# Kernel optimization log

Measured on AMD Instinct MI355X. Metric: run time of the kernel, lower is better.

## Reference

```python
import jax, jax.numpy as jnp
import numpy as np

N_EMBD = 1024
N_HEADS = 16
HEAD_SIZE = N_EMBD // N_HEADS
B, T = 2, 2048


def setup_inputs() -> dict:
    key = jax.random.key(0)
    ks = jax.random.split(key, 6)
    s_in = 1.0 / np.sqrt(N_EMBD)
    x = jax.random.normal(ks[0], (B, T, N_EMBD), dtype=jnp.float32)
    # per-head projection weights, stored (H, C, Dh) = x @ W per head
    wq = jax.random.uniform(ks[1], (N_HEADS, N_EMBD, HEAD_SIZE), dtype=jnp.float32, minval=-s_in, maxval=s_in)
    wk = jax.random.uniform(ks[2], (N_HEADS, N_EMBD, HEAD_SIZE), dtype=jnp.float32, minval=-s_in, maxval=s_in)
    wv = jax.random.uniform(ks[3], (N_HEADS, N_EMBD, HEAD_SIZE), dtype=jnp.float32, minval=-s_in, maxval=s_in)
    # output projection (in, out) layout plus bias
    w_proj = jax.random.uniform(ks[4], (N_EMBD, N_EMBD), dtype=jnp.float32, minval=-s_in, maxval=s_in)
    b_proj = jax.random.uniform(ks[5], (N_EMBD,), dtype=jnp.float32, minval=-s_in, maxval=s_in)
    return {"x": x, "wq": wq, "wk": wk, "wv": wv, "w_proj": w_proj, "b_proj": b_proj}


def reference(x, wq, wk, wv, w_proj, b_proj):
    Bb, Tt, C = x.shape
    # all-head QKV projections in one einsum each: (B,T,C)x(H,C,Dh)->(B,H,T,Dh)
    q = jnp.einsum('btc,hcd->bhtd', x, wq)
    k = jnp.einsum('btc,hcd->bhtd', x, wk)
    v = jnp.einsum('btc,hcd->bhtd', x, wv)
    # NOTE: original scales by C**-0.5 with C = full n_embd, not head_size
    scores = jnp.einsum('bhtd,bhsd->bhts', q, k) * (C ** -0.5)
    causal = jnp.tril(jnp.ones((Tt, Tt), dtype=bool))  # is_decoder=True
    scores = jnp.where(causal, scores, -jnp.inf)
    wei = jax.nn.softmax(scores, axis=-1)
    out = jnp.einsum('bhts,bhsd->bhtd', wei, v)
    # concat heads: (B,H,T,Dh) -> (B,T,H*Dh)
    out = out.transpose(0, 2, 1, 3).reshape(Bb, Tt, C)
    return out @ w_proj + b_proj
```

## Files before the change

kernel.cpp:

```cpp
#include <hip/hip_runtime.h>


typedef unsigned short u16;
typedef unsigned int u32;

using bf16x8 = __attribute__((ext_vector_type(8))) short;
using bf16x4 = __attribute__((ext_vector_type(4))) short;
using f32x4  = __attribute__((ext_vector_type(4))) float;

#define T_SEQ 2048
#define C_DIM 1024
#define H_NUM 16
#define D_HEAD 64
#define NSEG 41

static __device__ inline f32x4 mfma16(bf16x8 a, bf16x8 b, f32x4 c) {
  return __builtin_amdgcn_mfma_f32_16x16x32_bf16(a, b, c, 0, 0, 0);
}

static __device__ inline short f2bf(float f) {
  union { float f; u32 u; } v; v.f = f;
  u32 u = v.u;
  return (short)((u + 0x7FFFu + ((u >> 16) & 1u)) >> 16);
}

static __device__ inline float bf2f(short s) {
  union { u32 u; float f; } v; v.u = ((u32)(u16)s) << 16;
  return v.f;
}

static __device__ inline float exp2_hw(float x) {
  return __builtin_amdgcn_exp2f(x);
}

static __device__ inline u32 cvtpk_bf16(float a, float b) {
  u32 r;
  asm("v_cvt_pk_bf16_f32 %0, %1, %2" : "=v"(r) : "v"(a), "v"(b));
  return r;
}

static __device__ inline void gload_lds16(const short* g, short* l) {
  __builtin_amdgcn_global_load_lds(
      (const __attribute__((address_space(1))) unsigned int*)g,
      (__attribute__((address_space(3))) unsigned int*)l,
      16, 0, 0);
}

__global__ __launch_bounds__(256) void ingest_kernel(
    const float* __restrict__ x, const float* __restrict__ wq,
    const float* __restrict__ wk, const float* __restrict__ wv,
    const float* __restrict__ wproj,
    short* __restrict__ xb, short* __restrict__ wt, short* __restrict__ wpT) {
  const int bid = blockIdx.x, t = threadIdx.x;
  if (bid < 4096) {
    size_t i4 = ((size_t)bid * 256 + t) * 4;
    const float4 v = *(const float4*)(x + i4);
    bf16x4 o4;
    o4[0] = f2bf(v.x); o4[1] = f2bf(v.y); o4[2] = f2bf(v.z); o4[3] = f2bf(v.w);
    *(bf16x4*)(xb + i4) = o4;
    return;
  }
  __shared__ short lt[64][72];
  const int rl = t >> 2, q16 = (t & 3) * 16;
  if (bid < 4864) {
    const int wb = bid - 4096;
    const int h3 = wb >> 4, c0 = (wb & 15) * 64;
    const float* w = (h3 < 16) ? wq : (h3 < 32) ? wk : wv;
    const int h = h3 & 15;
    const float* rp = w + (size_t)h * 65536 + (size_t)(c0 + rl) * 64 + q16;
#pragma unroll
    for (int j = 0; j < 16; j++) lt[rl][q16 + j] = f2bf(rp[j]);
    __syncthreads();
    short* op = wt + (size_t)h3 * 65536 + (size_t)rl * 1024 + c0 + q16;
#pragma unroll
    for (int j = 0; j < 16; j++) op[j] = lt[q16 + j][rl];
  } else {
    const int wc = bid - 4864;
    const int k0 = (wc >> 4) * 64, n0 = (wc & 15) * 64;
    const float* rp = wproj + (size_t)(k0 + rl) * 1024 + n0 + q16;
#pragma unroll
    for (int j = 0; j < 16; j++) lt[rl][q16 + j] = f2bf(rp[j]);
    __syncthreads();
    short* op = wpT + (size_t)(n0 + rl) * 1024 + k0 + q16;
#pragma unroll
    for (int j = 0; j < 16; j++) op[j] = lt[q16 + j][rl];
  }
}

__global__ __launch_bounds__(256) void qkv_kernel(
    const short* __restrict__ x, const short* __restrict__ wt,
    short* __restrict__ qo, short* __restrict__ ko, short* __restrict__ vto) {
  const int m0 = blockIdx.x * 128;
  const int n0 = blockIdx.y * 128;
  const int tid = threadIdx.x, w = tid >> 6, lane = tid & 63;
  const int l15 = lane & 15, quad = lane >> 4;
  const int wm = w >> 1, wn = w & 1;

  __shared__ __align__(16) short As[2][128 * 32];
  __shared__ __align__(16) short Bs[2][128 * 32];

  const int srow = w * 32 + (lane >> 2);
  const int skof = (lane & 3) * 8;
  const short* ga0 = x  + (size_t)(m0 + srow) * 1024 + skof;
  const short* ga1 = ga0 + 16 * 1024;
  const short* gb0 = wt + (size_t)(n0 + srow) * 1024 + skof;
  const short* gb1 = gb0 + 16 * 1024;
  const int lof0 = (w * 32) * 32;
  const int lof1 = (w * 32 + 16) * 32;

  f32x4 acc[4][4];
#pragma unroll
  for (int i = 0; i < 4; i++)
#pragma unroll
    for (int j = 0; j < 4; j++) acc[i][j] = f32x4{0, 0, 0, 0};

  const bool isv = (n0 >= 2048);

  auto stage = [&](int bi, int kt) {
    const int k0 = kt * 32;
    gload_lds16(ga0 + k0, &As[bi][lof0]);
    gload_lds16(ga1 + k0, &As[bi][lof1]);
    gload_lds16(gb0 + k0, &Bs[bi][lof0]);
    gload_lds16(gb1 + k0, &Bs[bi][lof1]);
  };
  auto compute = [&](int bi) {
    const short* ard = &As[bi][(wm * 64 + l15) * 32 + quad * 8];
    const short* brd = &Bs[bi][(wn * 64 + l15) * 32 + quad * 8];
    bf16x8 af[4], bfr[4];
#pragma unroll
    for (int i = 0; i < 4; i++) {
      af[i]  = *(const bf16x8*)(ard + i * 16 * 32);
      bfr[i] = *(const bf16x8*)(brd + i * 16 * 32);
    }
    if (!isv) {
#pragma unroll
      for (int mi = 0; mi < 4; mi++)
#pragma unroll
        for (int ni = 0; ni < 4; ni++)
          acc[mi][ni] = mfma16(af[mi], bfr[ni], acc[mi][ni]);
    } else {
#pragma unroll
      for (int ni = 0; ni < 4; ni++)
#pragma unroll
        for (int mi = 0; mi < 4; mi++)
          acc[ni][mi] = mfma16(bfr[ni], af[mi], acc[ni][mi]);
    }
  };

  stage(0, 0);
  __syncthreads();
#pragma unroll 1
  for (int kt2 = 0; kt2 < 16; kt2++) {
    stage(1, 2 * kt2 + 1);
    compute(0);
    __syncthreads();
    if (kt2 < 15) stage(0, 2 * kt2 + 2);
    compute(1);
    __syncthreads();
  }

  const int chunk = (n0 >> 6) + wn;
  const int sel = chunk >> 4, h = chunk & 15;
  if (!isv) {
    short* outp = (sel == 0) ? qo : ko;
    const float sc = (sel == 0) ? 0.045084441f : 1.0f;
#pragma unroll
    for (int mi = 0; mi < 4; mi++) {
#pragma unroll
      for (int r = 0; r < 4; r++) {
        int tg = m0 + wm * 64 + mi * 16 + quad * 4 + r;
        int b = tg >> 11, tl = tg & 2047;
        size_t rowb = ((size_t)(b * H_NUM + h) * T_SEQ + tl) * D_HEAD;
#pragma unroll
        for (int ni = 0; ni < 4; ni++)
          outp[rowb + ni * 16 + l15] = f2bf(acc[mi][ni][r] * sc);
      }
    }
  } else {
#pragma unroll
    for (int ni = 0; ni < 4; ni++) {
#pragma unroll
      for (int r = 0; r < 4; r++) {
        int d = ni * 16 + quad * 4 + r;
#pragma unroll
        for (int mi = 0; mi < 4; mi++) {
          int tg = m0 + wm * 64 + mi * 16 + l15;
          int b = tg >> 11, tl = tg & 2047;
          vto[((size_t)(b * H_NUM + h) * D_HEAD + d) * T_SEQ + tl] =
              f2bf(acc[ni][mi][r]);
        }
      }
    }
  }
}

__global__ __launch_bounds__(128) void attn_part_kernel(
    const short* __restrict__ q, const short* __restrict__ k,
    const short* __restrict__ vt, short* __restrict__ po,
    float* __restrict__ pl) {
  static const unsigned char cst[33] = {
      0, 3, 5, 7, 9, 11, 12, 14, 15, 16, 17, 18, 19, 21, 22, 23, 24,
      25, 26, 27, 28, 29, 30, 31, 32, 34, 35, 36, 37, 38, 39, 40, 41};
  static const unsigned char seg_qtb[NSEG] = {
      0, 1, 2, 2, 3, 3, 4, 4, 5, 5, 6, 6, 6, 7, 7, 8, 8, 9, 9, 9,
      10, 10, 10, 11, 11, 11, 12, 12, 12, 13, 13, 13, 13, 14, 14, 14, 14,
      15, 15, 15, 15};
  static const unsigned short seg_s0[NSEG] = {
      0, 0, 0, 192, 0, 384, 0, 448, 0, 384, 0, 192, 768, 0, 448, 0, 576,
      0, 576, 1152, 0, 384, 896, 0, 512, 1024, 0, 576, 1152, 0, 576, 1152,
      1664, 0, 384, 896, 1408, 0, 512, 1024, 1536};
  static const unsigned char seg_nt[NSEG] = {
      2, 4, 3, 3, 6, 2, 7, 3, 6, 6, 3, 9, 2, 7, 9, 9, 9, 9, 9, 2,
      6, 8, 8, 8, 8, 8, 9, 9, 8, 9, 9, 8, 2, 6, 8, 8, 8, 8, 8, 8, 8};

  const int id = blockIdx.x;
  const int hb = id & 31;
  const int p  = id >> 5;
  const int pair = p & 1, chunk = p >> 1;

  const size_t bh = (size_t)hb;
  const short* qp = q  + bh * T_SEQ * D_HEAD;
  const short* kp = k  + bh * T_SEQ * D_HEAD;
  const short* vp = vt + bh * D_HEAD * T_SEQ;

  const int tid = threadIdx.x;
  const int wid = tid >> 6;
  const int lane = tid & 63;
  const int l15 = lane & 15, quad = lane >> 4;
  const int w4 = pair * 2 + wid;

  __shared__ __align__(16) short P_lds[2][32][72];
  short (*pq)[72] = P_lds[wid];

  const int sfirst = cst[chunk], slast = cst[chunk + 1];
#pragma unroll 1
  for (int si = sfirst; si < slast; ++si) {
    const int qtb = seg_qtb[si];
    const int sbeg = seg_s0[si];
    const int send = sbeg + seg_nt[si] * 64;
    const int q0w = qtb * 128 + w4 * 32;
    const int s_hi = min(send, ((q0w + 95) >> 6) << 6);

    bf16x8 qa[2][2];
#pragma unroll
    for (int h2 = 0; h2 < 2; h2++)
#pragma unroll
      for (int c2 = 0; c2 < 2; c2++)
        qa[h2][c2] = *(const bf16x8*)(qp + (size_t)(q0w + h2 * 16 + l15) * D_HEAD
                                      + c2 * 32 + quad * 8);

    f32x4 o[2][4];
#pragma unroll
    for (int h2 = 0; h2 < 2; h2++)
#pragma unroll
      for (int c = 0; c < 4; c++) o[h2][c] = f32x4{0, 0, 0, 0};
    float l_i[2] = { 0.f, 0.f };

    bf16x8 ka[4][2];
#pragma unroll
    for (int c = 0; c < 4; c++) {
      const short* krow = kp + (size_t)(sbeg + c * 16 + l15) * D_HEAD + quad * 8;
      ka[c][0] = *(const bf16x8*)(krow);
      ka[c][1] = *(const bf16x8*)(krow + 32);
    }

#pragma unroll 1
    for (int s0 = sbeg; s0 < s_hi; s0 += 64) {
      bf16x8 va[2][4];
#pragma unroll
      for (int kb2 = 0; kb2 < 2; kb2++)
#pragma unroll
        for (int c = 0; c < 4; c++)
          va[kb2][c] = *(const bf16x8*)(vp + (size_t)(c * 16 + l15) * T_SEQ
                                        + s0 + kb2 * 32 + quad * 8);

      f32x4 s[2][4];
      __builtin_amdgcn_s_setprio(1);
#pragma unroll
      for (int c = 0; c < 4; c++) {
#pragma unroll
        for (int h2 = 0; h2 < 2; h2++) {
          f32x4 z = { 0, 0, 0, 0 };
          z = mfma16(ka[c][0], qa[h2][0], z);
          z = mfma16(ka[c][1], qa[h2][1], z);
          s[h2][c] = z;
        }
      }
      __builtin_amdgcn_s_setprio(0);

      const int s0n = (s0 + 64 < s_hi) ? (s0 + 64) : s0;
#pragma unroll
      for (int c = 0; c < 4; c++) {
        const short* krow = kp + (size_t)(s0n + c * 16 + l15) * D_HEAD + quad * 8;
        ka[c][0] = *(const bf16x8*)(krow);
        ka[c][1] = *(const bf16x8*)(krow + 32);
      }

      const bool needMask = (s0 + 64 > q0w);
#pragma unroll
      for (int h2 = 0; h2 < 2; h2++) {
        const int qg = q0w + h2 * 16 + l15;
        if (needMask) {
#pragma unroll
          for (int c = 0; c < 4; c++)
#pragma unroll
            for (int r = 0; r < 4; r++)
              if (s0 + c * 16 + quad * 4 + r > qg) s[h2][c][r] = -1e30f;
        }
        float rs = 0.f;
#pragma unroll
        for (int c = 0; c < 4; c++) {
#pragma unroll
          for (int r = 0; r < 4; r++) {
            float p2 = exp2_hw(s[h2][c][r]);
            s[h2][c][r] = p2;
            rs += p2;
          }
        }
        l_i[h2] += rs;
#pragma unroll
        for (int c = 0; c < 4; c++) {
          uint2 pw;
          pw.x = cvtpk_bf16(s[h2][c][0], s[h2][c][1]);
          pw.y = cvtpk_bf16(s[h2][c][2], s[h2][c][3]);
          *(uint2*)(&pq[h2 * 16 + l15][c * 16 + quad * 4]) = pw;
        }
      }
      asm volatile("" ::: "memory");

      __builtin_amdgcn_s_setprio(1);
#pragma unroll
      for (int kb2 = 0; kb2 < 2; kb2++) {
        bf16x8 pb[2];
        pb[0] = *(const bf16x8*)(&pq[l15][kb2 * 32 + quad * 8]);
        pb[1] = *(const bf16x8*)(&pq[16 + l15][kb2 * 32 + quad * 8]);
#pragma unroll
        for (int c = 0; c < 4; c++) {
          o[0][c] = mfma16(va[kb2][c], pb[0], o[0][c]);
          o[1][c] = mfma16(va[kb2][c], pb[1], o[1][c]);
        }
      }
      __builtin_amdgcn_s_setprio(0);
      asm volatile("" ::: "memory");
    }

    const size_t prow = (bh * NSEG + si) * 128;
#pragma unroll
    for (int h2 = 0; h2 < 2; h2++) {
      float lsum = l_i[h2];
      lsum += __shfl_xor(lsum, 16);
      lsum += __shfl_xor(lsum, 32);
      float inv = (lsum > 0.f) ? 1.0f / lsum : 0.f;
      int qlocal = w4 * 32 + h2 * 16 + l15;
      size_t rowoff = (prow + qlocal) * 64;
#pragma unroll
      for (int c = 0; c < 4; c++) {
        uint2 ow;
        ow.x = cvtpk_bf16(o[h2][c][0] * inv, o[h2][c][1] * inv);
        ow.y = cvtpk_bf16(o[h2][c][2] * inv, o[h2][c][3] * inv);
        *(uint2*)(&po[rowoff + c * 16 + quad * 4]) = ow;
      }
      if (quad == 0) pl[prow + qlocal] = lsum;
    }
  }
}

__global__ __launch_bounds__(256) void attn_merge_kernel(
    const short* __restrict__ po, const float* __restrict__ pl,
    short* __restrict__ attnb) {
  static const unsigned char mseg0[16] = {0, 1, 2, 4, 6, 8, 10, 13,
                                          15, 17, 20, 23, 26, 29, 33, 37};
  static const unsigned char mcnt[16]  = {1, 1, 2, 2, 2, 2, 3, 2,
                                          2, 3, 3, 3, 3, 4, 4, 4};
  int id = blockIdx.x * 256 + threadIdx.x;
  int dg = id & 7;
  int h  = (id >> 3) & 15;
  int t  = (id >> 7) & 2047;
  int b  = id >> 18;
  int qtb = t >> 7, ql = t & 127;
  int nch = mcnt[qtb];
  size_t bh = (size_t)(b * H_NUM + h);
  size_t r0 = (bh * NSEG + mseg0[qtb]) * 128 + ql;
  bf16x8 res;
  if (nch == 1) {
    res = *(const bf16x8*)(po + r0 * 64 + dg * 8);
  } else {
    float acc[8] = {0, 0, 0, 0, 0, 0, 0, 0};
    float lsum = 0.f;
    for (int c = 0; c < nch; c++) {
      size_t r = r0 + (size_t)c * 128;
      float lc = pl[r];
      lsum += lc;
      bf16x8 p = *(const bf16x8*)(po + r * 64 + dg * 8);
#pragma unroll
      for (int j = 0; j < 8; j++) acc[j] += lc * bf2f(p[j]);
    }
    float inv = 1.0f / lsum;
#pragma unroll
    for (int j = 0; j < 8; j++) res[j] = f2bf(acc[j] * inv);
  }
  *(bf16x8*)(&attnb[((size_t)(b * T_SEQ + t)) * C_DIM + h * D_HEAD + dg * 8]) = res;
}

__global__ __launch_bounds__(256) void proj_kernel(
    const short* __restrict__ a_in, const short* __restrict__ wpT,
    const float* __restrict__ bias, float* __restrict__ out) {
  const int m0 = blockIdx.x * 128;
  const int n0 = blockIdx.y * 128;
  const int tid = threadIdx.x, w = tid >> 6, lane = tid & 63;
  const int l15 = lane & 15, quad = lane >> 4;
  const int wm = w >> 1, wn = w & 1;

  __shared__ __align__(16) short As[2][128 * 32];
  __shared__ __align__(16) short Bs[2][128 * 32];

  const int srow = w * 32 + (lane >> 2);
  const int skof = (lane & 3) * 8;
  const short* ga0 = a_in + (size_t)(m0 + srow) * 1024 + skof;
  const short* ga1 = ga0 + 16 * 1024;
  const short* gb0 = wpT + (size_t)(n0 + srow) * 1024 + skof;
  const short* gb1 = gb0 + 16 * 1024;
  const int lof0 = (w * 32) * 32;
  const int lof1 = (w * 32 + 16) * 32;

  f32x4 acc[4][4];
#pragma unroll
  for (int i = 0; i < 4; i++)
#pragma unroll
    for (int j = 0; j < 4; j++) acc[i][j] = f32x4{0, 0, 0, 0};

  auto stage = [&](int bi, int kt) {
    const int k0 = kt * 32;
    gload_lds16(ga0 + k0, &As[bi][lof0]);
    gload_lds16(ga1 + k0, &As[bi][lof1]);
    gload_lds16(gb0 + k0, &Bs[bi][lof0]);
    gload_lds16(gb1 + k0, &Bs[bi][lof1]);
  };
  auto compute = [&](int bi) {
    const short* ard = &As[bi][(wm * 64 + l15) * 32 + quad * 8];
    const short* brd = &Bs[bi][(wn * 64 + l15) * 32 + quad * 8];
    bf16x8 af[4], bfr[4];
#pragma unroll
    for (int i = 0; i < 4; i++) {
      af[i]  = *(const bf16x8*)(ard + i * 16 * 32);
      bfr[i] = *(const bf16x8*)(brd + i * 16 * 32);
    }
#pragma unroll
    for (int mi = 0; mi < 4; mi++)
#pragma unroll
      for (int ni = 0; ni < 4; ni++)
        acc[mi][ni] = mfma16(af[mi], bfr[ni], acc[mi][ni]);
  };

  stage(0, 0);
  __syncthreads();
#pragma unroll 1
  for (int kt2 = 0; kt2 < 16; kt2++) {
    stage(1, 2 * kt2 + 1);
    compute(0);
    __syncthreads();
    if (kt2 < 15) stage(0, 2 * kt2 + 2);
    compute(1);
    __syncthreads();
  }

#pragma unroll
  for (int mi = 0; mi < 4; mi++) {
#pragma unroll
    for (int r = 0; r < 4; r++) {
      int mq = m0 + wm * 64 + mi * 16 + quad * 4 + r;
#pragma unroll
      for (int ni = 0; ni < 4; ni++) {
        int n = n0 + wn * 64 + ni * 16 + l15;
        out[(size_t)mq * C_DIM + n] = acc[mi][ni][r] + bias[n];
      }
    }
  }
}

extern "C" void kernel_launch(void* const* d_in, const int* in_sizes, int n_in,
                              void* d_out, int out_size, void* d_ws, size_t ws_size,
                              hipStream_t stream) {
  const float* x     = (const float*)d_in[0];
  const float* wq    = (const float*)d_in[1];
  const float* wk    = (const float*)d_in[2];
  const float* wv    = (const float*)d_in[3];
  const float* wproj = (const float*)d_in[4];
  const float* bias  = (const float*)d_in[5];

  short* ws = (short*)d_ws;
  short* wpT    = ws;
  short* qb     = ws + 1048576;
  short* wt_qkv = ws + 9437184;
  short* xb     = ws + 12582912;
  short* po     = ws + 5242880;
  float* pl     = (float*)(ws + 15990784);
  short* attnb  = ws + 1048576;
  short* kb     = (short*)d_out;
  short* vtb    = (short*)d_out + 4194304;

  ingest_kernel<<<5120, 256, 0, stream>>>(x, wq, wk, wv, wproj, xb, wt_qkv, wpT);
  qkv_kernel<<<dim3(32, 24), 256, 0, stream>>>(xb, wt_qkv, qb, kb, vtb);
  attn_part_kernel<<<2048, 128, 0, stream>>>(qb, kb, vtb, po, pl);
  attn_merge_kernel<<<2048, 256, 0, stream>>>(po, pl, attnb);
  proj_kernel<<<dim3(32, 8), 256, 0, stream>>>(attnb, wpT, bias, (float*)d_out);
}
```

Measured before the change: 232.5 us.

## Stage K/V tiles in shared memory across four waves with uniform 512-key chunks

The attention-partial kernel now runs 4-wave blocks that cover a whole 128-query tile. Each 64-key K and V tile is loaded into swizzled LDS with direct global-to-LDS loads and shared by all waves, where before each wave fetched K and V from global memory itself. The split into work items changes from a hand-tuned segment table to fixed 512-key chunks, dispatched in a heavy-first order, and the merge kernel's indexing is updated to match. This cuts redundant global K/V traffic, at the cost of two block barriers per tile and less per-wave freedom to run independently.

```diff
diff --git a/kernel.cpp b/kernel.cpp
--- a/kernel.cpp
+++ b/kernel.cpp
@@ -12,7 +12,7 @@
 #define C_DIM 1024
 #define H_NUM 16
 #define D_HEAD 64
-#define NSEG 41
+#define NCHUNK 40
 
 static __device__ inline f32x4 mfma16(bf16x8 a, bf16x8 b, f32x4 c) {
   return __builtin_amdgcn_mfma_f32_16x16x32_bf16(a, b, c, 0, 0, 0);
@@ -194,29 +194,29 @@
   }
 }
 
-__global__ __launch_bounds__(128) void attn_part_kernel(
+__global__ __launch_bounds__(256) void attn_part_kernel(
     const short* __restrict__ q, const short* __restrict__ k,
     const short* __restrict__ vt, short* __restrict__ po,
     float* __restrict__ pl) {
-  static const unsigned char cst[33] = {
-      0, 3, 5, 7, 9, 11, 12, 14, 15, 16, 17, 18, 19, 21, 22, 23, 24,
-      25, 26, 27, 28, 29, 30, 31, 32, 34, 35, 36, 37, 38, 39, 40, 41};
-  static const unsigned char seg_qtb[NSEG] = {
-      0, 1, 2, 2, 3, 3, 4, 4, 5, 5, 6, 6, 6, 7, 7, 8, 8, 9, 9, 9,
-      10, 10, 10, 11, 11, 11, 12, 12, 12, 13, 13, 13, 13, 14, 14, 14, 14,
+  static const unsigned char order[NCHUNK] = {
+      3, 4, 6, 8, 10, 11, 12, 13, 15, 16, 18, 19, 21, 22, 23, 24, 25, 26,
+      28, 29, 30, 32, 33, 34, 36, 37, 38, 39,
+      2, 9, 20, 35,
+      1, 7, 17, 31,
+      0, 5, 14, 27};
+  static const unsigned char qtb_of[NCHUNK] = {
+      0, 1, 2, 3, 4, 4, 5, 5, 6, 6, 7, 7, 8, 8, 8, 9, 9, 9, 10, 10,
+      10, 11, 11, 11, 12, 12, 12, 12, 13, 13, 13, 13, 14, 14, 14, 14,
       15, 15, 15, 15};
-  static const unsigned short seg_s0[NSEG] = {
-      0, 0, 0, 192, 0, 384, 0, 448, 0, 384, 0, 192, 768, 0, 448, 0, 576,
-      0, 576, 1152, 0, 384, 896, 0, 512, 1024, 0, 576, 1152, 0, 576, 1152,
-      1664, 0, 384, 896, 1408, 0, 512, 1024, 1536};
-  static const unsigned char seg_nt[NSEG] = {
-      2, 4, 3, 3, 6, 2, 7, 3, 6, 6, 3, 9, 2, 7, 9, 9, 9, 9, 9, 2,
-      6, 8, 8, 8, 8, 8, 9, 9, 8, 9, 9, 8, 2, 6, 8, 8, 8, 8, 8, 8, 8};
-
+  static const unsigned char base16[16] = {0, 1, 2, 3, 4, 6, 8, 10,
+                                           12, 15, 18, 21, 24, 28, 32, 36};
   const int id = blockIdx.x;
   const int hb = id & 31;
   const int p  = id >> 5;
-  const int pair = p & 1, chunk = p >> 1;
+  const int pblk = order[p];
+  const int qtb = qtb_of[pblk];
+  const int sbeg = (pblk - base16[qtb]) * 512;
+  const int send = min(sbeg + 512, (qtb + 1) * 128);
 
   const size_t bh = (size_t)hb;
   const short* qp = q  + bh * T_SEQ * D_HEAD;
@@ -224,163 +224,163 @@
   const short* vp = vt + bh * D_HEAD * T_SEQ;
 
   const int tid = threadIdx.x;
-  const int wid = tid >> 6;
+  const int w4 = tid >> 6;
   const int lane = tid & 63;
   const int l15 = lane & 15, quad = lane >> 4;
-  const int w4 = pair * 2 + wid;
-
-  __shared__ __align__(16) short P_lds[2][32][72];
-  short (*pq)[72] = P_lds[wid];
-
-  const int sfirst = cst[chunk], slast = cst[chunk + 1];
+  const int swz8 = (l15 & 7) * 8;
+
+  __shared__ __align__(16) short Ks[4096];
+  __shared__ __align__(16) short Vs[4096];
+  __shared__ __align__(16) short Ps[4][2048];
+  short* pp = Ps[w4];
+
+  const int q0w = qtb * 128 + w4 * 32;
+  const int s_hi = min(send, ((qtb * 128 + 96 + 95) >> 6) << 6);
+
+  const int srow = w4 * 16 + (lane >> 3);
+  const int scol = ((lane & 7) ^ (lane >> 3)) * 8;
+  const short* gK0 = kp + (size_t)(sbeg + srow) * 64 + scol;
+  const short* gK1 = kp + (size_t)(sbeg + srow + 8) * 64 + scol;
+  const short* gV0 = vp + (size_t)srow * 2048 + sbeg + scol;
+  const short* gV1 = vp + (size_t)(srow + 8) * 2048 + sbeg + scol;
+  short* lK0 = Ks + w4 * 1024 + lane * 8;
+  short* lK1 = Ks + w4 * 1024 + 512 + lane * 8;
+  short* lV0 = Vs + w4 * 1024 + lane * 8;
+  short* lV1 = Vs + w4 * 1024 + 512 + lane * 8;
+
+  auto stageKV = [&](int toff) {
+    gload_lds16(gK0 + (size_t)toff * 64, lK0);
+    gload_lds16(gK1 + (size_t)toff * 64, lK1);
+    gload_lds16(gV0 + toff, lV0);
+    gload_lds16(gV1 + toff, lV1);
+  };
+
+  const int rbase = l15 * 64;
+  const int koff0 = (quad * 8) ^ swz8;
+  const int koff1 = (32 + quad * 8) ^ swz8;
+
+  bf16x8 qa[2][2];
+#pragma unroll
+  for (int h2 = 0; h2 < 2; h2++)
+#pragma unroll
+    for (int c2 = 0; c2 < 2; c2++)
+      qa[h2][c2] = *(const bf16x8*)(qp + (size_t)(q0w + h2 * 16 + l15) * D_HEAD
+                                    + c2 * 32 + quad * 8);
+
+  f32x4 o[2][4];
+#pragma unroll
+  for (int h2 = 0; h2 < 2; h2++)
+#pragma unroll
+    for (int c = 0; c < 4; c++) o[h2][c] = f32x4{0, 0, 0, 0};
+  float l_i[2] = { 0.f, 0.f };
+
+  stageKV(0);
+
 #pragma unroll 1
-  for (int si = sfirst; si < slast; ++si) {
-    const int qtb = seg_qtb[si];
-    const int sbeg = seg_s0[si];
-    const int send = sbeg + seg_nt[si] * 64;
-    const int q0w = qtb * 128 + w4 * 32;
-    const int s_hi = min(send, ((q0w + 95) >> 6) << 6);
-
-    bf16x8 qa[2][2];
-#pragma unroll
-    for (int h2 = 0; h2 < 2; h2++)
-#pragma unroll
-      for (int c2 = 0; c2 < 2; c2++)
-        qa[h2][c2] = *(const bf16x8*)(qp + (size_t)(q0w + h2 * 16 + l15) * D_HEAD
-                                      + c2 * 32 + quad * 8);
-
-    f32x4 o[2][4];
-#pragma unroll
-    for (int h2 = 0; h2 < 2; h2++)
-#pragma unroll
-      for (int c = 0; c < 4; c++) o[h2][c] = f32x4{0, 0, 0, 0};
-    float l_i[2] = { 0.f, 0.f };
-
-    bf16x8 ka[4][2];
+  for (int s0 = sbeg; s0 < s_hi; s0 += 64) {
+    __syncthreads();
+
+    f32x4 s[2][4];
+    __builtin_amdgcn_s_setprio(1);
 #pragma unroll
     for (int c = 0; c < 4; c++) {
-      const short* krow = kp + (size_t)(sbeg + c * 16 + l15) * D_HEAD + quad * 8;
-      ka[c][0] = *(const bf16x8*)(krow);
-      ka[c][1] = *(const bf16x8*)(krow + 32);
-    }
-
-#pragma unroll 1
-    for (int s0 = sbeg; s0 < s_hi; s0 += 64) {
-      bf16x8 va[2][4];
-#pragma unroll
-      for (int kb2 = 0; kb2 < 2; kb2++)
+      bf16x8 k0 = *(const bf16x8*)(Ks + c * 1024 + rbase + koff0);
+      bf16x8 k1 = *(const bf16x8*)(Ks + c * 1024 + rbase + koff1);
+#pragma unroll
+      for (int h2 = 0; h2 < 2; h2++) {
+        f32x4 z = { 0, 0, 0, 0 };
+        z = mfma16(k0, qa[h2][0], z);
+        z = mfma16(k1, qa[h2][1], z);
+        s[h2][c] = z;
+      }
+    }
+    __builtin_amdgcn_s_setprio(0);
+
+    const bool needMask = (s0 + 64 > q0w);
+#pragma unroll
+    for (int h2 = 0; h2 < 2; h2++) {
+      const int qg = q0w + h2 * 16 + l15;
+      if (needMask) {
 #pragma unroll
         for (int c = 0; c < 4; c++)
-          va[kb2][c] = *(const bf16x8*)(vp + (size_t)(c * 16 + l15) * T_SEQ
-                                        + s0 + kb2 * 32 + quad * 8);
-
-      f32x4 s[2][4];
-      __builtin_amdgcn_s_setprio(1);
+#pragma unroll
+          for (int r = 0; r < 4; r++)
+            if (s0 + c * 16 + quad * 4 + r > qg) s[h2][c][r] = -1e30f;
+      }
+      float rs = 0.f;
 #pragma unroll
       for (int c = 0; c < 4; c++) {
 #pragma unroll
-        for (int h2 = 0; h2 < 2; h2++) {
-          f32x4 z = { 0, 0, 0, 0 };
-          z = mfma16(ka[c][0], qa[h2][0], z);
-          z = mfma16(ka[c][1], qa[h2][1], z);
-          s[h2][c] = z;
+        for (int r = 0; r < 4; r++) {
+          float p2 = exp2_hw(s[h2][c][r]);
+          s[h2][c][r] = p2;
+          rs += p2;
         }
       }
-      __builtin_amdgcn_s_setprio(0);
-
-      const int s0n = (s0 + 64 < s_hi) ? (s0 + 64) : s0;
+      l_i[h2] += rs;
 #pragma unroll
       for (int c = 0; c < 4; c++) {
-        const short* krow = kp + (size_t)(s0n + c * 16 + l15) * D_HEAD + quad * 8;
-        ka[c][0] = *(const bf16x8*)(krow);
-        ka[c][1] = *(const bf16x8*)(krow + 32);
-      }
-
-      const bool needMask = (s0 + 64 > q0w);
-#pragma unroll
-      for (int h2 = 0; h2 < 2; h2++) {
-        const int qg = q0w + h2 * 16 + l15;
-        if (needMask) {
-#pragma unroll
-          for (int c = 0; c < 4; c++)
-#pragma unroll
-            for (int r = 0; r < 4; r++)
-              if (s0 + c * 16 + quad * 4 + r > qg) s[h2][c][r] = -1e30f;
-        }
-        float rs = 0.f;
-#pragma unroll
-        for (int c = 0; c < 4; c++) {
-#pragma unroll
-          for (int r = 0; r < 4; r++) {
-            float p2 = exp2_hw(s[h2][c][r]);
-            s[h2][c][r] = p2;
-            rs += p2;
-          }
-        }
-        l_i[h2] += rs;
-#pragma unroll
-        for (int c = 0; c < 4; c++) {
-          uint2 pw;
-          pw.x = cvtpk_bf16(s[h2][c][0], s[h2][c][1]);
-          pw.y = cvtpk_bf16(s[h2][c][2], s[h2][c][3]);
-          *(uint2*)(&pq[h2 * 16 + l15][c * 16 + quad * 4]) = pw;
-        }
-      }
-      asm volatile("" ::: "memory");
-
-      __builtin_amdgcn_s_setprio(1);
-#pragma unroll
-      for (int kb2 = 0; kb2 < 2; kb2++) {
-        bf16x8 pb[2];
-        pb[0] = *(const bf16x8*)(&pq[l15][kb2 * 32 + quad * 8]);
-        pb[1] = *(const bf16x8*)(&pq[16 + l15][kb2 * 32 + quad * 8]);
-#pragma unroll
-        for (int c = 0; c < 4; c++) {
-          o[0][c] = mfma16(va[kb2][c], pb[0], o[0][c]);
-          o[1][c] = mfma16(va[kb2][c], pb[1], o[1][c]);
-        }
-      }
-      __builtin_amdgcn_s_setprio(0);
-      asm volatile("" ::: "memory");
-    }
-
-    const size_t prow = (bh * NSEG + si) * 128;
-#pragma unroll
-    for (int h2 = 0; h2 < 2; h2++) {
-      float lsum = l_i[h2];
-      lsum += __shfl_xor(lsum, 16);
-      lsum += __shfl_xor(lsum, 32);
-      float inv = (lsum > 0.f) ? 1.0f / lsum : 0.f;
-      int qlocal = w4 * 32 + h2 * 16 + l15;
-      size_t rowoff = (prow + qlocal) * 64;
+        uint2 pw;
+        pw.x = cvtpk_bf16(s[h2][c][0], s[h2][c][1]);
+        pw.y = cvtpk_bf16(s[h2][c][2], s[h2][c][3]);
+        *(uint2*)(pp + (h2 * 16 + l15) * 64 + ((c * 16 + quad * 4) ^ swz8)) = pw;
+      }
+    }
+    asm volatile("" ::: "memory");
+
+    __builtin_amdgcn_s_setprio(1);
+#pragma unroll
+    for (int kb2 = 0; kb2 < 2; kb2++) {
+      const int ko = kb2 ? koff1 : koff0;
+      bf16x8 pb0 = *(const bf16x8*)(pp + rbase + ko);
+      bf16x8 pb1 = *(const bf16x8*)(pp + 1024 + rbase + ko);
 #pragma unroll
       for (int c = 0; c < 4; c++) {
-        uint2 ow;
-        ow.x = cvtpk_bf16(o[h2][c][0] * inv, o[h2][c][1] * inv);
-        ow.y = cvtpk_bf16(o[h2][c][2] * inv, o[h2][c][3] * inv);
-        *(uint2*)(&po[rowoff + c * 16 + quad * 4]) = ow;
-      }
-      if (quad == 0) pl[prow + qlocal] = lsum;
-    }
+        bf16x8 va = *(const bf16x8*)(Vs + c * 1024 + rbase + ko);
+        o[0][c] = mfma16(va, pb0, o[0][c]);
+        o[1][c] = mfma16(va, pb1, o[1][c]);
+      }
+    }
+    __builtin_amdgcn_s_setprio(0);
+
+    __syncthreads();
+    if (s0 + 64 < s_hi) stageKV(s0 + 64 - sbeg);
+  }
+
+  const size_t prow = (bh * NCHUNK + pblk) * 128;
+#pragma unroll
+  for (int h2 = 0; h2 < 2; h2++) {
+    float lsum = l_i[h2];
+    lsum += __shfl_xor(lsum, 16);
+    lsum += __shfl_xor(lsum, 32);
+    float inv = (lsum > 0.f) ? 1.0f / lsum : 0.f;
+    int qlocal = w4 * 32 + h2 * 16 + l15;
+    size_t rowoff = (prow + qlocal) * 64;
+#pragma unroll
+    for (int c = 0; c < 4; c++) {
+      uint2 ow;
+      ow.x = cvtpk_bf16(o[h2][c][0] * inv, o[h2][c][1] * inv);
+      ow.y = cvtpk_bf16(o[h2][c][2] * inv, o[h2][c][3] * inv);
+      *(uint2*)(&po[rowoff + c * 16 + quad * 4]) = ow;
+    }
+    if (quad == 0) pl[prow + qlocal] = lsum;
   }
 }
 
 __global__ __launch_bounds__(256) void attn_merge_kernel(
     const short* __restrict__ po, const float* __restrict__ pl,
     short* __restrict__ attnb) {
-  static const unsigned char mseg0[16] = {0, 1, 2, 4, 6, 8, 10, 13,
-                                          15, 17, 20, 23, 26, 29, 33, 37};
-  static const unsigned char mcnt[16]  = {1, 1, 2, 2, 2, 2, 3, 2,
-                                          2, 3, 3, 3, 3, 4, 4, 4};
+  static const unsigned char base16[16] = {0, 1, 2, 3, 4, 6, 8, 10,
+                                           12, 15, 18, 21, 24, 28, 32, 36};
   int id = blockIdx.x * 256 + threadIdx.x;
   int dg = id & 7;
   int h  = (id >> 3) & 15;
   int t  = (id >> 7) & 2047;
   int b  = id >> 18;
   int qtb = t >> 7, ql = t & 127;
-  int nch = mcnt[qtb];
+  int nch = (qtb >> 2) + 1;
   size_t bh = (size_t)(b * H_NUM + h);
-  size_t r0 = (bh * NSEG + mseg0[qtb]) * 128 + ql;
+  size_t r0 = (bh * NCHUNK + base16[qtb]) * 128 + ql;
   bf16x8 res;
   if (nch == 1) {
     res = *(const bf16x8*)(po + r0 * 64 + dg * 8);
@@ -494,14 +494,14 @@
   short* wt_qkv = ws + 9437184;
   short* xb     = ws + 12582912;
   short* po     = ws + 5242880;
-  float* pl     = (float*)(ws + 15990784);
+  float* pl     = (float*)(ws + 15728640);
   short* attnb  = ws + 1048576;
   short* kb     = (short*)d_out;
   short* vtb    = (short*)d_out + 4194304;
 
   ingest_kernel<<<5120, 256, 0, stream>>>(x, wq, wk, wv, wproj, xb, wt_qkv, wpT);
   qkv_kernel<<<dim3(32, 24), 256, 0, stream>>>(xb, wt_qkv, qb, kb, vtb);
-  attn_part_kernel<<<2048, 128, 0, stream>>>(qb, kb, vtb, po, pl);
+  attn_part_kernel<<<NCHUNK * 32, 256, 0, stream>>>(qb, kb, vtb, po, pl);
   attn_merge_kernel<<<2048, 256, 0, stream>>>(po, pl, attnb);
   proj_kernel<<<dim3(32, 8), 256, 0, stream>>>(attnb, wpT, bias, (float*)d_out);
 }
```

After: 196.4 us. 15.5% less time.
